# Optimization experiments

Measured on AMD Instinct MI355X. Metric: run time of the kernel, lower is better.

Reference implementation:

```python
import jax, jax.numpy as jnp
import numpy as np

HIDDEN = 4096
N_HEADS = 32
N_KV_HEADS = 8
HEAD_DIM = HIDDEN // N_HEADS  # 128
N_KV_GROUPS = N_HEADS // N_KV_HEADS  # 4
SEQ = 2048
BSZ = 1
ROPE_THETA = 10000.0


def _rope_cos_sin(seqlen, head_dim, dtype):
    # freqs_cis = polar(1, outer(t, theta^{-2i/d})) -> cos/sin tables [S, hd/2]
    inv_freq = 1.0 / (ROPE_THETA ** (jnp.arange(0, head_dim, 2, dtype=jnp.float32) / head_dim))
    t = jnp.arange(seqlen, dtype=jnp.float32)
    freqs = jnp.outer(t, inv_freq)  # [S, hd/2]
    return jnp.cos(freqs).astype(dtype), jnp.sin(freqs).astype(dtype)


def _apply_rotary(x, cos, sin):
    # x: [B, S, H, hd]. Torch code pairs (x[:hd/2], x[hd/2:]) as (real, imag):
    # out = concat(x1*cos - x2*sin, x1*sin + x2*cos)
    half = x.shape[-1] // 2
    x1, x2 = x[..., :half], x[..., half:]
    c = cos[None, :, None, :]  # [1, S, 1, hd/2]
    s = sin[None, :, None, :]
    return jnp.concatenate([x1 * c - x2 * s, x1 * s + x2 * c], axis=-1)


def setup_inputs() -> dict:
    key = jax.random.key(0)
    k1, k2, k3 = jax.random.split(key, 3)
    hidden_states = jax.random.normal(k1, (BSZ, SEQ, HIDDEN), dtype=jnp.float32)
    w_qkv = jax.random.normal(k2, (HIDDEN, (N_HEADS + 2 * N_KV_HEADS) * HEAD_DIM), dtype=jnp.float32) * 0.02
    w_o = jax.random.normal(k3, (HIDDEN, HIDDEN), dtype=jnp.float32) * 0.02
    # HF-style additive causal mask [1, 1, S, S]
    causal = jnp.tril(jnp.ones((SEQ, SEQ), dtype=bool))
    attention_mask = jnp.where(causal, 0.0, -1e9).astype(jnp.float32)[None, None]
    return {"hidden_states": hidden_states, "w_qkv": w_qkv, "w_o": w_o,
            "attention_mask": attention_mask}


def reference(hidden_states, w_qkv, w_o, attention_mask):
    bsz, seqlen, _ = hidden_states.shape
    # fused (dequantized) QKV projection
    xqkv = jnp.einsum('bsh,hd->bsd', hidden_states, w_qkv)
    xqkv = xqkv.reshape(bsz, seqlen, N_HEADS + 2 * N_KV_HEADS, HEAD_DIM)
    xq = xqkv[:, :, :N_HEADS]                      # [B, S, 32, 128]
    xk = xqkv[:, :, N_HEADS:N_HEADS + N_KV_HEADS]  # [B, S, 8, 128]
    xv = xqkv[:, :, -N_KV_HEADS:]                  # [B, S, 8, 128]

    cos, sin = _rope_cos_sin(seqlen, HEAD_DIM, hidden_states.dtype)
    xq = _apply_rotary(xq, cos, sin)
    xk = _apply_rotary(xk, cos, sin)

    # GQA: repeat_interleave kv heads along head dim
    keys = jnp.repeat(xk, N_KV_GROUPS, axis=2)    # [B, S, 32, 128]
    values = jnp.repeat(xv, N_KV_GROUPS, axis=2)

    q = xq.transpose(0, 2, 1, 3)   # [B, H, S, D]
    k = keys.transpose(0, 2, 1, 3)
    v = values.transpose(0, 2, 1, 3)

    scores = jnp.einsum('bhqd,bhkd->bhqk', q, k) / np.sqrt(HEAD_DIM)
    scores = scores + attention_mask
    probs = jax.nn.softmax(scores.astype(jnp.float32), axis=-1).astype(q.dtype)
    out = jnp.einsum('bhqk,bhkd->bhqd', probs, v)
    attention_weight = out.transpose(0, 2, 1, 3).reshape(bsz, seqlen, -1)
    attn_output = jnp.einsum('bsh,ho->bso', attention_weight, w_o)
    return attn_output
```

## Files before the change

kernel.cpp:

```cpp
#include <hip/hip_runtime.h>
#include <stdint.h>

typedef unsigned short u16;
typedef __bf16 bf8 __attribute__((ext_vector_type(8)));
typedef float f32x4 __attribute__((ext_vector_type(4)));

#define SEQ 2048
#define HIDDEN 4096
#define DQKV 6144
#define HD 128

#define GLOAD_LDS16(g, l)                                                            \
    __builtin_amdgcn_global_load_lds((const __attribute__((address_space(1))) void*)(g), \
                                     (__attribute__((address_space(3))) void*)(l), 16, 0, 0)

__device__ __forceinline__ u16 f2bf(float f) {
    union { float f; unsigned u; } v{f};
    unsigned r = (v.u + 0x7fff + ((v.u >> 16) & 1)) >> 16;
    return (u16)r;
}
__device__ __forceinline__ float bf2f(u16 b) {
    union { unsigned u; float f; } v;
    v.u = ((unsigned)b) << 16;
    return v.f;
}


__global__ void convert_bf16_kernel(const float* __restrict__ in, u16* __restrict__ out) {
    int i = (blockIdx.x * 256 + threadIdx.x) * 4;
    float4 v = *(const float4*)(in + i);
    u16 o[4] = {f2bf(v.x), f2bf(v.y), f2bf(v.z), f2bf(v.w)};
    *(uint2*)(out + i) = *(uint2*)o;
}

__global__ void transpose_w_kernel(const float* __restrict__ in, u16* __restrict__ out, int K, int N) {
    __shared__ u16 tile[64][65];
    int tn = N >> 6;
    int bk = blockIdx.x / tn, bn = blockIdx.x % tn;
    int k0 = bk * 64, n0 = bn * 64;
    int c = threadIdx.x & 63, r0 = threadIdx.x >> 6;
#pragma unroll
    for (int r = r0; r < 64; r += 4)
        tile[r][c] = f2bf(in[(size_t)(k0 + r) * N + n0 + c]);
    __syncthreads();
#pragma unroll
    for (int r = r0; r < 64; r += 4)
        out[(size_t)(n0 + r) * K + k0 + c] = tile[c][r];
}

__global__ void rope_kernel(u16* __restrict__ x) {
    const int row = blockIdx.x / 10, hg = blockIdx.x % 10;
    const int head = hg * 4 + (threadIdx.x >> 6), j = threadIdx.x & 63;
    u16* p = x + (size_t)row * DQKV + head * HD + j;
    float x1 = bf2f(p[0]), x2 = bf2f(p[64]);
    float inv = exp2f(-(float)j * 0.20762050593045952f);
    float s, c;
    sincosf((float)row * inv, &s, &c);
    p[0] = f2bf(x1 * c - x2 * s);
    p[64] = f2bf(x1 * s + x2 * c);
}

__global__ void transpose_v_kernel(const u16* __restrict__ xqkv, u16* __restrict__ vt) {
    __shared__ u16 tile[64][65];
    int h = blockIdx.x >> 6;
    int t = blockIdx.x & 63;
    int s0 = (t >> 1) * 64, d0 = (t & 1) * 64;
    int c = threadIdx.x & 63, r0 = threadIdx.x >> 6;
    const u16* src = xqkv + (40 + h) * HD + d0;
#pragma unroll
    for (int r = r0; r < 64; r += 4)
        tile[r][c] = src[(size_t)(s0 + r) * DQKV + c];
    __syncthreads();
    u16* dst = vt + ((size_t)h * HD + d0) * SEQ + s0;
#pragma unroll
    for (int r = r0; r < 64; r += 4)
        dst[(size_t)r * SEQ + c] = tile[c][r];
}

template <int BM, int BN, int MODE>
__global__ __launch_bounds__(512, 2) void gemm8p_kernel(const u16* __restrict__ A,
                                                        const u16* __restrict__ BT,
                                                        u16* __restrict__ Cbf,
                                                        float* __restrict__ Cf) {
    constexpr int WM = BM / 32;
    constexpr int WN = BN / 64;
    constexpr int MP = WM / 4;
    constexpr int NLA = BM / 64, NLB = BN / 64, NL = NLA + NLB;
    constexpr int NBN = ((MODE == 0) ? DQKV : HIDDEN) / BN;
    constexpr int NBM = SEQ / BM;
    constexpr int CSTR = (MODE == 0) ? DQKV : HIDDEN;
    constexpr int NT = 64;
    static_assert(NBM * NBN == 256, "grid must be exactly 256 blocks");
    __shared__ __align__(16) u16 lds[2][(BM + BN) * 64];

    const int tid = threadIdx.x;
    const int w = tid >> 6, l = tid & 63, l15 = l & 15, q4 = l >> 4;
    const int wm = w >> 2, wn = w & 3;

    const int xcd = blockIdx.x & 7, wi = blockIdx.x >> 3;
    int bm, bn;
    if constexpr (NBN == 32) {
        bm = (xcd >> 2) * 4 + (wi >> 3);
        bn = (xcd & 3) * 8 + (wi & 7);
    } else {
        bm = (xcd & 3) * 4 + (wi >> 3);
        bn = (xcd >> 2) * 8 + (wi & 7);
    }

    const int srow = tid >> 3;
    const int scol = ((tid & 7) ^ ((tid >> 3) & 7)) << 4;
    const char* spA[NLA];
    const char* spB[NLB];
#pragma unroll
    for (int L = 0; L < NLA; ++L)
        spA[L] = (const char*)(A + (size_t)(bm * BM + L * 64 + srow) * 4096) + scol;
#pragma unroll
    for (int L = 0; L < NLB; ++L)
        spB[L] = (const char*)(BT + (size_t)(bn * BN + L * 64 + srow) * 4096) + scol;

#define STG_A(L, tt, b) GLOAD_LDS16(spA[L] + (size_t)(tt) * 128, &lds[b][(L) * 4096 + w * 512])
#define STG_B(L, tt, b) GLOAD_LDS16(spB[L] + (size_t)(tt) * 128, &lds[b][BM * 64 + (L) * 4096 + w * 512])

#pragma unroll
    for (int L = 0; L < NLA; ++L) STG_A(L, 0, 0);
#pragma unroll
    for (int L = 0; L < NLB; ++L) STG_B(L, 0, 0);
#pragma unroll
    for (int L = 0; L < NLA; ++L) STG_A(L, 1, 1);
#pragma unroll
    for (int L = 0; L < NLB; ++L) STG_B(L, 1, 1);
    if constexpr (NL == 7) asm volatile("s_waitcnt vmcnt(7)" ::: "memory");
    else                   asm volatile("s_waitcnt vmcnt(6)" ::: "memory");
    asm volatile("s_barrier" ::: "memory");

    const int c0x = (q4 * 16) ^ ((l15 & 7) << 4);
    const int c1x = c0x ^ 64;

    f32x4 acc[WM][WN] = {};
    bf8 breg[WN][2];

#pragma unroll 1
    for (int t = 0; t < NT; ++t) {
        const int cur = t & 1;
        const char* ldsA = (const char*)&lds[cur][0];
        const char* ldsB = ldsA + BM * 128;
#pragma unroll
        for (int p = 0; p < 4; ++p) {
            if (p == 1 && t < NT - 2) {
#pragma unroll
                for (int L = 0; L < NLB; ++L) STG_B(L, t + 2, cur);
            }
            if constexpr (BM == 256) {
                if (p == 2 && t < NT - 2) {
                    STG_A(0, t + 2, cur);
                    STG_A(2, t + 2, cur);
                }
            }
            bf8 areg[MP][2];
#pragma unroll
            for (int j = 0; j < MP; ++j) {
                const char* rp = ldsA + (wm * (BM / 2) + (p * MP + j) * 16 + l15) * 128;
                areg[j][0] = *(const bf8*)(rp + c0x);
                areg[j][1] = *(const bf8*)(rp + c1x);
            }
            if (p == 0) {
#pragma unroll
                for (int nf = 0; nf < WN; ++nf) {
                    const char* rp = ldsB + (wn * (WN * 16) + nf * 16 + l15) * 128;
                    breg[nf][0] = *(const bf8*)(rp + c0x);
                    breg[nf][1] = *(const bf8*)(rp + c1x);
                }
            }
            asm volatile("s_barrier" ::: "memory");
            asm volatile("s_waitcnt lgkmcnt(0)" ::: "memory");
            __builtin_amdgcn_s_setprio(1);
#pragma unroll
            for (int j = 0; j < MP; ++j)
#pragma unroll
                for (int nf = 0; nf < WN; ++nf)
#pragma unroll
                    for (int ks = 0; ks < 2; ++ks)
                        acc[p * MP + j][nf] = __builtin_amdgcn_mfma_f32_16x16x32_bf16(
                            areg[j][ks], breg[nf][ks], acc[p * MP + j][nf], 0, 0, 0);
            __builtin_amdgcn_s_setprio(0);
            asm volatile("s_barrier" ::: "memory");
        }
        if (t < NT - 2) {
            if constexpr (BM == 256) { STG_A(1, t + 2, cur); STG_A(3, t + 2, cur); }
            else                     { STG_A(0, t + 2, cur); STG_A(1, t + 2, cur); }
            if constexpr (NL == 7) asm volatile("s_waitcnt vmcnt(7)" ::: "memory");
            else                   asm volatile("s_waitcnt vmcnt(6)" ::: "memory");
        } else if (t == NT - 2) {
            asm volatile("s_waitcnt vmcnt(0)" ::: "memory");
        }
        asm volatile("s_barrier" ::: "memory");
    }
#undef STG_A
#undef STG_B

    const int rowb = bm * BM + wm * (BM / 2);
    const int colb = bn * BN + wn * (WN * 16);
#pragma unroll
    for (int mf = 0; mf < WM; ++mf)
#pragma unroll
        for (int nf = 0; nf < WN; ++nf)
#pragma unroll
            for (int r = 0; r < 4; ++r) {
                const int row = rowb + mf * 16 + q4 * 4 + r;
                const int col = colb + nf * 16 + l15;
                if constexpr (MODE == 0)
                    Cbf[(size_t)row * CSTR + col] = f2bf(acc[mf][nf][r]);
                else
                    Cf[(size_t)row * CSTR + col] = acc[mf][nf][r];
            }
}

#define PSTR 72
__global__ __launch_bounds__(256) void attn_kernel(const u16* __restrict__ xqkv,
                                                   const u16* __restrict__ vt,
                                                   u16* __restrict__ aw) {
    __shared__ __align__(16) u16 sm[16384 + 128 * PSTR];
    const int tid = threadIdx.x, w = tid >> 6, l = tid & 63, l15 = l & 15, q4 = l >> 4;
    const int qh = blockIdx.x & 31;
    const int qslot = blockIdx.x >> 5;
    const int qt = (qslot < 8) ? qslot : 23 - qslot;
    const int kh = qh >> 2;

    {
        const u16* gq = xqkv + (size_t)(qt * 128 + (l >> 2)) * DQKV + qh * HD + w * 32 + (l & 3) * 8;
#pragma unroll
        for (int i = 0; i < 8; ++i)
            GLOAD_LDS16(gq + (size_t)i * 16 * DQKV, &sm[w * 4096 + i * 512]);
    }
    __syncthreads();
    bf8 qf[4][2];
#pragma unroll
    for (int ks = 0; ks < 4; ++ks)
#pragma unroll
        for (int mt = 0; mt < 2; ++mt)
            qf[ks][mt] = *(const bf8*)&sm[ks * 4096 + (w * 32 + mt * 16 + l15) * 32 + q4 * 8];
    __syncthreads();

    f32x4 O[2][8] = {};
    float plrow[2][4] = {};

    u16* ldsK = sm;
    u16* ldsV = sm + 8192;
    u16* ldsP = sm + 16384;
    const int nkt = 2 * qt + 2;
    const float cs = 0.12751744f;

    const u16* gk_base = xqkv + (32 + kh) * HD + w * 32 + (l & 3) * 8;
    const u16* gv_base = vt + (size_t)kh * HD * SEQ + (size_t)((w & 1) * 64 + (l >> 2)) * SEQ + (w >> 1) * 32 + (l & 3) * 8;

    for (int kt = 0; kt < nkt; ++kt) {
        {
            const u16* gk = gk_base + (size_t)(kt * 64 + (l >> 2)) * DQKV;
#pragma unroll
            for (int i = 0; i < 4; ++i)
                GLOAD_LDS16(gk + (size_t)i * 16 * DQKV, ldsK + w * 2048 + i * 512);
        }
        {
            const u16* gv = gv_base + kt * 64;
#pragma unroll
            for (int i = 0; i < 4; ++i)
                GLOAD_LDS16(gv + (size_t)i * 16 * SEQ, ldsV + (w >> 1) * 4096 + (w & 1) * 2048 + i * 512);
        }
        __syncthreads();

        f32x4 S[2][4] = {};
#pragma unroll
        for (int ks = 0; ks < 4; ++ks) {
            bf8 kf[4];
#pragma unroll
            for (int nt = 0; nt < 4; ++nt)
                kf[nt] = *(const bf8*)&ldsK[ks * 2048 + (nt * 16 + l15) * 32 + q4 * 8];
#pragma unroll
            for (int mt = 0; mt < 2; ++mt)
#pragma unroll
                for (int nt = 0; nt < 4; ++nt)
                    S[mt][nt] = __builtin_amdgcn_mfma_f32_16x16x32_bf16(qf[ks][mt], kf[nt], S[mt][nt], 0, 0, 0);
        }

        const bool domask = (kt >= 2 * qt);
#pragma unroll
        for (int mt = 0; mt < 2; ++mt)
#pragma unroll
            for (int r = 0; r < 4; ++r) {
                const int row = qt * 128 + w * 32 + mt * 16 + q4 * 4 + r;
#pragma unroll
                for (int nt = 0; nt < 4; ++nt) {
                    float t = S[mt][nt][r] * cs;
                    if (domask && (kt * 64 + nt * 16 + l15 > row)) t = -1e30f;
                    float p = exp2f(t);
                    plrow[mt][r] += p;
                    ldsP[(w * 32 + mt * 16 + q4 * 4 + r) * PSTR + nt * 16 + l15] = f2bf(p);
                }
            }

#pragma unroll
        for (int pk = 0; pk < 2; ++pk) {
            bf8 pf[2], vf[8];
#pragma unroll
            for (int mt = 0; mt < 2; ++mt)
                pf[mt] = *(const bf8*)&ldsP[(w * 32 + mt * 16 + l15) * PSTR + pk * 32 + q4 * 8];
#pragma unroll
            for (int nt = 0; nt < 8; ++nt)
                vf[nt] = *(const bf8*)&ldsV[pk * 4096 + (nt * 16 + l15) * 32 + q4 * 8];
#pragma unroll
            for (int mt = 0; mt < 2; ++mt)
#pragma unroll
                for (int nt = 0; nt < 8; ++nt)
                    O[mt][nt] = __builtin_amdgcn_mfma_f32_16x16x32_bf16(pf[mt], vf[nt], O[mt][nt], 0, 0, 0);
        }
        __syncthreads();
    }

#pragma unroll
    for (int mt = 0; mt < 2; ++mt)
#pragma unroll
        for (int r = 0; r < 4; ++r) {
            float ls = plrow[mt][r];
#pragma unroll
            for (int off = 1; off <= 8; off <<= 1)
                ls += __shfl_xor(ls, off, 64);
            const float linv = 1.0f / ls;
            const int row = qt * 128 + w * 32 + mt * 16 + q4 * 4 + r;
#pragma unroll
            for (int nt = 0; nt < 8; ++nt)
                aw[(size_t)row * 4096 + qh * HD + nt * 16 + l15] = f2bf(O[mt][nt][r] * linv);
        }
}


extern "C" void kernel_launch(void* const* d_in, const int* in_sizes, int n_in,
                              void* d_out, int out_size, void* d_ws, size_t ws_size,
                              hipStream_t stream) {
    const float* hs = (const float*)d_in[0];
    const float* wqkv = (const float*)d_in[1];
    const float* wo = (const float*)d_in[2];
    float* out = (float*)d_out;

    char* ws = (char*)d_ws;
    const size_t oHbf = 0;
    const size_t oWqkvT = oHbf + (size_t)SEQ * HIDDEN * 2;
    const size_t oWoT = oWqkvT + (size_t)DQKV * HIDDEN * 2;
    const size_t oXQKV = oWoT + (size_t)HIDDEN * HIDDEN * 2;
    const size_t oVT = oXQKV + (size_t)SEQ * DQKV * 2;
    const size_t oAW = oVT + (size_t)8 * HD * SEQ * 2;
    const size_t total = oAW + (size_t)SEQ * HIDDEN * 2;
    if (ws_size < total) return;

    u16* Hbf = (u16*)(ws + oHbf);
    u16* WqkvT = (u16*)(ws + oWqkvT);
    u16* WoT = (u16*)(ws + oWoT);
    u16* XQKV = (u16*)(ws + oXQKV);
    u16* VT = (u16*)(ws + oVT);
    u16* AW = (u16*)(ws + oAW);

    convert_bf16_kernel<<<(SEQ * HIDDEN) / 1024, 256, 0, stream>>>(hs, Hbf);
    transpose_w_kernel<<<(HIDDEN / 64) * (DQKV / 64), 256, 0, stream>>>(wqkv, WqkvT, HIDDEN, DQKV);
    transpose_w_kernel<<<(HIDDEN / 64) * (HIDDEN / 64), 256, 0, stream>>>(wo, WoT, HIDDEN, HIDDEN);
    gemm8p_kernel<256, 192, 0><<<256, 512, 0, stream>>>(Hbf, WqkvT, XQKV, nullptr);
    rope_kernel<<<SEQ * 10, 256, 0, stream>>>(XQKV);
    transpose_v_kernel<<<8 * 64, 256, 0, stream>>>(XQKV, VT);
    attn_kernel<<<512, 256, 0, stream>>>(XQKV, VT, AW);
    gemm8p_kernel<128, 256, 1><<<256, 512, 0, stream>>>(AW, WoT, nullptr, out);
}
```

Before: 523.3 us.

## Reshape GEMM wave grid per mode and swizzle attention K/V LDS tiles

The GEMM's wave arrangement now depends on mode: the QKV projection uses a 4x2 wave grid and the output projection keeps 4x4, with A-tile staging consolidated into a single loop after the compute phases. The attention kernel changes K and V global-to-LDS loads to contiguous 128-byte rows, using an XOR column swizzle to avoid LDS bank conflicts on fragment reads. The aim is fewer LDS bank conflicts and better global load coalescing. Moving all A staging to the end of the iteration could reduce overlap between loads and MFMA work.

```diff
diff --git a/kernel.cpp b/kernel.cpp
--- a/kernel.cpp
+++ b/kernel.cpp
@@ -82,9 +82,11 @@
                                                         const u16* __restrict__ BT,
                                                         u16* __restrict__ Cbf,
                                                         float* __restrict__ Cf) {
-    constexpr int WM = BM / 32;
-    constexpr int WN = BN / 64;
+    constexpr int WAVES_N = (MODE == 0) ? 2 : 4;
+    constexpr int WM = BM * WAVES_N / 128;
+    constexpr int WN = BN / (WAVES_N * 16);
     constexpr int MP = WM / 4;
+    static_assert(WM >= 4 && MP >= 1, "wave split arithmetic");
     constexpr int NLA = BM / 64, NLB = BN / 64, NL = NLA + NLB;
     constexpr int NBN = ((MODE == 0) ? DQKV : HIDDEN) / BN;
     constexpr int NBM = SEQ / BM;
@@ -95,7 +97,7 @@
 
     const int tid = threadIdx.x;
     const int w = tid >> 6, l = tid & 63, l15 = l & 15, q4 = l >> 4;
-    const int wm = w >> 2, wn = w & 3;
+    const int wm = w / WAVES_N, wn = w % WAVES_N;
 
     const int xcd = blockIdx.x & 7, wi = blockIdx.x >> 3;
     int bm, bn;
@@ -150,16 +152,10 @@
 #pragma unroll
                 for (int L = 0; L < NLB; ++L) STG_B(L, t + 2, cur);
             }
-            if constexpr (BM == 256) {
-                if (p == 2 && t < NT - 2) {
-                    STG_A(0, t + 2, cur);
-                    STG_A(2, t + 2, cur);
-                }
-            }
             bf8 areg[MP][2];
 #pragma unroll
             for (int j = 0; j < MP; ++j) {
-                const char* rp = ldsA + (wm * (BM / 2) + (p * MP + j) * 16 + l15) * 128;
+                const char* rp = ldsA + (wm * (WM * 16) + (p * MP + j) * 16 + l15) * 128;
                 areg[j][0] = *(const bf8*)(rp + c0x);
                 areg[j][1] = *(const bf8*)(rp + c1x);
             }
@@ -186,8 +182,8 @@
             asm volatile("s_barrier" ::: "memory");
         }
         if (t < NT - 2) {
-            if constexpr (BM == 256) { STG_A(1, t + 2, cur); STG_A(3, t + 2, cur); }
-            else                     { STG_A(0, t + 2, cur); STG_A(1, t + 2, cur); }
+#pragma unroll
+            for (int L = 0; L < NLA; ++L) STG_A(L, t + 2, cur);
             if constexpr (NL == 7) asm volatile("s_waitcnt vmcnt(7)" ::: "memory");
             else                   asm volatile("s_waitcnt vmcnt(6)" ::: "memory");
         } else if (t == NT - 2) {
@@ -198,7 +194,7 @@
 #undef STG_A
 #undef STG_B
 
-    const int rowb = bm * BM + wm * (BM / 2);
+    const int rowb = bm * BM + wm * (WM * 16);
     const int colb = bn * BN + wn * (WN * 16);
 #pragma unroll
     for (int mf = 0; mf < WM; ++mf)
@@ -250,21 +246,29 @@
     const int nkt = 2 * qt + 2;
     const float cs = 0.12751744f;
 
-    const u16* gk_base = xqkv + (32 + kh) * HD + w * 32 + (l & 3) * 8;
-    const u16* gv_base = vt + (size_t)kh * HD * SEQ + (size_t)((w & 1) * 64 + (l >> 2)) * SEQ + (w >> 1) * 32 + (l & 3) * 8;
+    const int sr8 = l >> 3;
+    const int sc8 = (l & 7) ^ sr8;
+    const u16* gk_base = xqkv + (size_t)((w >> 1) * 32 + sr8) * DQKV + (32 + kh) * HD + (w & 1) * 64 + sc8 * 8;
+    u16* ldsK_dst = ldsK + (w & 1) * 4096 + (w >> 1) * 2048;
+    const u16* gv_base = vt + ((size_t)kh * HD + w * 32 + sr8) * SEQ + sc8 * 8;
+    u16* ldsV_dst = ldsV + w * 2048;
+
+    const int cswz = (q4 ^ (l15 & 7)) << 4;
+    const char* Kb = (const char*)ldsK;
+    const char* Vb = (const char*)ldsV;
 
     for (int kt = 0; kt < nkt; ++kt) {
         {
-            const u16* gk = gk_base + (size_t)(kt * 64 + (l >> 2)) * DQKV;
+            const u16* gk = gk_base + (size_t)(kt * 64) * DQKV;
 #pragma unroll
             for (int i = 0; i < 4; ++i)
-                GLOAD_LDS16(gk + (size_t)i * 16 * DQKV, ldsK + w * 2048 + i * 512);
+                GLOAD_LDS16(gk + (size_t)i * 8 * DQKV, ldsK_dst + i * 512);
         }
         {
             const u16* gv = gv_base + kt * 64;
 #pragma unroll
             for (int i = 0; i < 4; ++i)
-                GLOAD_LDS16(gv + (size_t)i * 16 * SEQ, ldsV + (w >> 1) * 4096 + (w & 1) * 2048 + i * 512);
+                GLOAD_LDS16(gv + (size_t)i * 8 * SEQ, ldsV_dst + i * 512);
         }
         __syncthreads();
 
@@ -274,7 +278,8 @@
             bf8 kf[4];
 #pragma unroll
             for (int nt = 0; nt < 4; ++nt)
-                kf[nt] = *(const bf8*)&ldsK[ks * 2048 + (nt * 16 + l15) * 32 + q4 * 8];
+                kf[nt] = *(const bf8*)(Kb + (ks >> 1) * 8192 + (nt * 16 + l15) * 128
+                                       + (cswz ^ ((ks & 1) << 6)));
 #pragma unroll
             for (int mt = 0; mt < 2; ++mt)
 #pragma unroll
@@ -306,7 +311,7 @@
                 pf[mt] = *(const bf8*)&ldsP[(w * 32 + mt * 16 + l15) * PSTR + pk * 32 + q4 * 8];
 #pragma unroll
             for (int nt = 0; nt < 8; ++nt)
-                vf[nt] = *(const bf8*)&ldsV[pk * 4096 + (nt * 16 + l15) * 32 + q4 * 8];
+                vf[nt] = *(const bf8*)(Vb + (nt * 16 + l15) * 128 + (cswz ^ (pk << 6)));
 #pragma unroll
             for (int mt = 0; mt < 2; ++mt)
 #pragma unroll
```

Measured after the change: 524.7 us. No clear change (+0.3%).
